# Kernel tuning notes

Hardware: AMD Instinct MI355X
Metric: run time of the kernel (lower is better)

## Reference

```python
import jax, jax.numpy as jnp
import numpy as np
import math

NUM_HEADS = 16
VEC_SIZE = 1024
HEAD_DIM = VEC_SIZE // NUM_HEADS


def setup_inputs() -> dict:
    key = jax.random.key(0)
    k1, k2, k3, k4, k5 = jax.random.split(key, 5)
    B, S, D = 2, 2048, VEC_SIZE
    x = jax.random.normal(k1, (B, S, D), dtype=jnp.float32)
    # Linear params, torch-style: y = x @ W.T + b
    s1 = 1.0 / math.sqrt(D)
    W_qkv = jax.random.uniform(k2, (3 * D, D), minval=-s1, maxval=s1, dtype=jnp.float32)
    b_qkv = jax.random.uniform(k3, (3 * D,), minval=-s1, maxval=s1, dtype=jnp.float32)
    W_out = jax.random.uniform(k4, (D, D), minval=-s1, maxval=s1, dtype=jnp.float32)
    b_out = jax.random.uniform(k5, (D,), minval=-s1, maxval=s1, dtype=jnp.float32)
    return {"x": x, "W_qkv": W_qkv, "b_qkv": b_qkv, "W_out": W_out, "b_out": b_out}


def reference(x, W_qkv, b_qkv, W_out, b_out):
    B, S, D = x.shape
    H, Hd = NUM_HEADS, HEAD_DIM
    qkv = x @ W_qkv.T + b_qkv                      # [B,S,3D]
    q, k, v = jnp.split(qkv, 3, axis=-1)
    # [B,S,H,Hd] -> [B,H,S,Hd]
    q = q.reshape(B, S, H, Hd).transpose(0, 2, 1, 3)
    k = k.reshape(B, S, H, Hd).transpose(0, 2, 1, 3)
    v = v.reshape(B, S, H, Hd).transpose(0, 2, 1, 3)
    weight = jnp.einsum('bhqd,bhkd->bhqk', q, k)   # [B,H,S,S]
    causal = jnp.triu(jnp.ones((S, S), dtype=bool), k=1)
    weight = jnp.where(causal, -jnp.inf, weight)
    weight = weight / jnp.sqrt(jnp.asarray(Hd, dtype=weight.dtype))
    weight = jax.nn.softmax(weight, axis=-1)
    out = jnp.einsum('bhqk,bhkd->bhqd', weight, v)  # [B,H,S,Hd]
    out = out.transpose(0, 2, 1, 3).reshape(B, S, D)
    return out @ W_out.T + b_out
```

## Files before the change

kernel.cpp:

```cpp
#include <hip/hip_runtime.h>
#include <hip/hip_bf16.h>

typedef __attribute__((ext_vector_type(8))) short short8;
typedef __attribute__((ext_vector_type(4))) short s4v;
typedef __attribute__((ext_vector_type(4))) float floatx4;

__device__ inline floatx4 mfma_bf16(short8 a, short8 b, floatx4 c) {
  return __builtin_amdgcn_mfma_f32_16x16x32_bf16(a, b, c, 0, 0, 0);
}
__device__ inline float exp2_fast(float x) { return __builtin_amdgcn_exp2f(x); }

__device__ inline short bf16s(float f) {
  __hip_bfloat16 h = __float2bfloat16(f);
  return *reinterpret_cast<short*>(&h);
}
__device__ inline float sbf16(short s) {
  return __bfloat162float(*reinterpret_cast<__hip_bfloat16*>(&s));
}

__device__ inline void gld16(__hip_bfloat16* lds, const __hip_bfloat16* g) {
  __builtin_amdgcn_global_load_lds(
      (const __attribute__((address_space(1))) void*)g,
      (__attribute__((address_space(3))) void*)lds, 16, 0, 0);
}

__global__ __launch_bounds__(256) void cvt_all(
    const float* __restrict__ x, const float* __restrict__ wqkv,
    const float* __restrict__ wout, __hip_bfloat16* __restrict__ xb,
    __hip_bfloat16* __restrict__ wqkvb, __hip_bfloat16* __restrict__ wob) {
  const int n1 = 4194304, n2 = 3145728;
  int i = (blockIdx.x * 256 + threadIdx.x) * 8;
  const float* src;
  __hip_bfloat16* dst;
  int off;
  if (i < n1) { src = x; dst = xb; off = i; }
  else if (i < n1 + n2) { src = wqkv; dst = wqkvb; off = i - n1; }
  else { src = wout; dst = wob; off = i - n1 - n2; }
  float4 a = *reinterpret_cast<const float4*>(src + off);
  float4 b = *reinterpret_cast<const float4*>(src + off + 4);
  __hip_bfloat16 t[8];
  t[0] = __float2bfloat16(a.x); t[1] = __float2bfloat16(a.y);
  t[2] = __float2bfloat16(a.z); t[3] = __float2bfloat16(a.w);
  t[4] = __float2bfloat16(b.x); t[5] = __float2bfloat16(b.y);
  t[6] = __float2bfloat16(b.z); t[7] = __float2bfloat16(b.w);
  *reinterpret_cast<short8*>(dst + off) = *reinterpret_cast<short8*>(t);
}

template<int TN, bool OUT_BF16>
__global__ __launch_bounds__(256) void gemm_bt(
    const __hip_bfloat16* __restrict__ A, const __hip_bfloat16* __restrict__ Bt,
    const float* __restrict__ bias, void* __restrict__ Cout,
    int M, int N, int K) {
  __shared__ __align__(16) __hip_bfloat16 As[128 * 64];
  __shared__ __align__(16) __hip_bfloat16 Bs[TN * 64];
  const int tid = threadIdx.x;
  const int wave = tid >> 6, lane = tid & 63, quad = lane >> 4, l15 = lane & 15;
  const int wm = (wave >> 1) * 64, wn = (wave & 1) * (TN / 2);
  const int m0 = blockIdx.y * 128, n0 = blockIdx.x * TN;
  const int NC = TN / 32;

  floatx4 acc[4][NC];
  for (int r = 0; r < 4; ++r)
    for (int c = 0; c < NC; ++c) acc[r][c] = (floatx4){0.f, 0.f, 0.f, 0.f};

  for (int k0 = 0; k0 < K; k0 += 64) {
    __syncthreads();
    for (int it = 0; it < 4; ++it) {
      int idx = it * 256 + tid;
      int row = idx >> 3, col = ((idx & 7) ^ (row & 7)) * 8;
      gld16(&As[idx * 8], A + (size_t)(m0 + row) * K + k0 + col);
    }
    for (int it = 0; it < TN * 64 / 2048; ++it) {
      int idx = it * 256 + tid;
      int row = idx >> 3, col = ((idx & 7) ^ (row & 7)) * 8;
      gld16(&Bs[idx * 8], Bt + (size_t)(n0 + row) * K + k0 + col);
    }
    __syncthreads();
    for (int ks = 0; ks < 2; ++ks) {
      short8 af[4], bf[NC];
      for (int r = 0; r < 4; ++r) {
        int row = wm + r * 16 + l15;
        af[r] = *reinterpret_cast<const short8*>(
            &As[row * 64 + (((ks * 4 + quad) ^ (l15 & 7)) * 8)]);
      }
      for (int c = 0; c < NC; ++c) {
        int row = wn + c * 16 + l15;
        bf[c] = *reinterpret_cast<const short8*>(
            &Bs[row * 64 + (((ks * 4 + quad) ^ (l15 & 7)) * 8)]);
      }
      for (int r = 0; r < 4; ++r)
        for (int c = 0; c < NC; ++c)
          acc[r][c] = mfma_bf16(af[r], bf[c], acc[r][c]);
    }
  }

  for (int c = 0; c < NC; ++c) {
    int gn = n0 + wn + c * 16 + l15;
    float bv = bias[gn];
    for (int r = 0; r < 4; ++r)
      for (int rg = 0; rg < 4; ++rg) {
        int gm = m0 + wm + r * 16 + quad * 4 + rg;
        float v = acc[r][c][rg] + bv;
        if (OUT_BF16)
          ((__hip_bfloat16*)Cout)[(size_t)gm * N + gn] = __float2bfloat16(v);
        else
          ((float*)Cout)[(size_t)gm * N + gn] = v;
      }
  }
}

__device__ inline void stage_half(__hip_bfloat16* lds, const __hip_bfloat16* g,
                                  int K, int tid) {
#pragma unroll
  for (int it = 0; it < 2; ++it) {
    int idx = it * 512 + tid;
    int row = idx >> 3, col = ((idx & 7) ^ (row & 7)) * 8;
    gld16(lds + idx * 8, g + (size_t)row * K + col);
  }
}

#define VMW(N) asm volatile("s_waitcnt vmcnt(" #N ")" ::: "memory")
#define LGKM0 asm volatile("s_waitcnt lgkmcnt(0)" ::: "memory")
#define BAR __builtin_amdgcn_s_barrier()

#define LDA8(dst, BUF, MH)                                                     \
  do {                                                                         \
    _Pragma("unroll") for (int mf = 0; mf < 4; ++mf) {                         \
      int rh = wm * 64 + mf * 16 + l15;                                        \
      _Pragma("unroll") for (int ks = 0; ks < 2; ++ks)                         \
          dst[mf][ks] = *reinterpret_cast<const short8*>(                      \
              &SA[BUF][MH][rh * 64 + (((ks * 4 + quad) ^ (rh & 7)) * 8)]);     \
    }                                                                          \
  } while (0)
#define LDB4(dst, BUF, NH)                                                     \
  do {                                                                         \
    _Pragma("unroll") for (int nf = 0; nf < 2; ++nf) {                         \
      int rh = wn * 32 + nf * 16 + l15;                                        \
      _Pragma("unroll") for (int ks = 0; ks < 2; ++ks)                         \
          dst[nf][ks] = *reinterpret_cast<const short8*>(                      \
              &SB[BUF][NH][rh * 64 + (((ks * 4 + quad) ^ (rh & 7)) * 8)]);     \
    }                                                                          \
  } while (0)
#define MM16(MH, NH, AF, BF)                                                   \
  do {                                                                         \
    _Pragma("unroll") for (int mf = 0; mf < 4; ++mf)                           \
        _Pragma("unroll") for (int nf = 0; nf < 2; ++nf) {                     \
      acc[MH][NH][mf][nf] = mfma_bf16(AF[mf][0], BF[nf][0], acc[MH][NH][mf][nf]); \
      acc[MH][NH][mf][nf] = mfma_bf16(AF[mf][1], BF[nf][1], acc[MH][NH][mf][nf]); \
    }                                                                          \
  } while (0)
#define PH(RD, STG, MH, NH, AF, BF, WT)                                        \
  do {                                                                         \
    RD;                                                                        \
    STG;                                                                       \
    BAR;                                                                       \
    __builtin_amdgcn_s_setprio(1);                                             \
    MM16(MH, NH, AF, BF);                                                      \
    __builtin_amdgcn_s_setprio(0);                                             \
    WT;                                                                        \
    LGKM0;                                                                     \
    BAR;                                                                       \
  } while (0)

template<bool OUT_BF16>
__global__ __launch_bounds__(512, 2) void gemm_256(
    const __hip_bfloat16* __restrict__ A, const __hip_bfloat16* __restrict__ Bt,
    const float* __restrict__ bias, void* __restrict__ Cout,
    int M, int N, int K) {
  __shared__ __align__(16) __hip_bfloat16 SA[2][2][128 * 64];
  __shared__ __align__(16) __hip_bfloat16 SB[2][2][128 * 64];
  const int tid = threadIdx.x;
  const int lane = tid & 63, quad = (lane >> 4), l15 = lane & 15;
  const int wave = tid >> 6;
  const int wm = wave >> 2, wn = wave & 3;

  const int nbx = gridDim.x;
  int bid = blockIdx.y * nbx + blockIdx.x;
  const int nwg = nbx * gridDim.y;
  if ((nwg & 7) == 0) bid = (bid & 7) * (nwg >> 3) + (bid >> 3);
  const int bx = bid % nbx, by = bid / nbx;
  const int m0 = by * 256, n0 = bx * 256;

  const __hip_bfloat16* Abase = A + (size_t)m0 * K;
  const __hip_bfloat16* Bbase = Bt + (size_t)n0 * K;
  const int NT = K >> 6;

  floatx4 acc[2][2][4][2];
#pragma unroll
  for (int a = 0; a < 2; ++a)
#pragma unroll
    for (int b = 0; b < 2; ++b)
#pragma unroll
      for (int c = 0; c < 4; ++c)
#pragma unroll
        for (int d = 0; d < 2; ++d) acc[a][b][c][d] = (floatx4){0.f, 0.f, 0.f, 0.f};

  short8 af0[4][2], af1[4][2];
  short8 bf0c[2][2], bf0n[2][2];
  short8 bf1[2][2];

  stage_half(&SB[0][0][0], Bbase, K, tid);
  stage_half(&SA[0][0][0], Abase, K, tid);
  stage_half(&SB[0][1][0], Bbase + (size_t)128 * K, K, tid);
  stage_half(&SA[0][1][0], Abase + (size_t)128 * K, K, tid);
  stage_half(&SB[1][0][0], Bbase + 64, K, tid);
  stage_half(&SA[1][0][0], Abase + 64, K, tid);
  stage_half(&SB[1][1][0], Bbase + (size_t)128 * K + 64, K, tid);
  stage_half(&SA[1][1][0], Abase + (size_t)128 * K + 64, K, tid);
  VMW(12);
  BAR;
  LDB4(bf0c, 0, 0);
  LDA8(af0, 0, 0);
  VMW(10);
  LGKM0;
  BAR;

  for (int t = 0; t <= NT - 3; ++t) {
    const int cb = t & 1, nb = cb ^ 1;
    const size_t k2 = (size_t)(t + 2) * 64;
    PH(LDB4(bf1, cb, 1), stage_half(&SB[cb][0][0], Bbase + k2, K, tid),
       0, 0, af0, bf0c, VMW(10));
    PH(LDA8(af1, cb, 1), stage_half(&SA[cb][0][0], Abase + k2, K, tid),
       0, 1, af0, bf1, VMW(10));
    PH(LDB4(bf0n, nb, 0),
       stage_half(&SB[cb][1][0], Bbase + (size_t)128 * K + k2, K, tid),
       1, 1, af1, bf1, VMW(10));
    PH(LDA8(af0, nb, 0),
       stage_half(&SA[cb][1][0], Abase + (size_t)128 * K + k2, K, tid),
       1, 0, af1, bf0c, VMW(10));
#pragma unroll
    for (int nf = 0; nf < 2; ++nf)
#pragma unroll
      for (int ks = 0; ks < 2; ++ks) bf0c[nf][ks] = bf0n[nf][ks];
  }
  {
    const int cb = (NT - 2) & 1, nb = cb ^ 1;
    PH(LDB4(bf1, cb, 1), (void)0, 0, 0, af0, bf0c, VMW(8));
    PH(LDA8(af1, cb, 1), (void)0, 0, 1, af0, bf1, VMW(6));
    PH(LDB4(bf0n, nb, 0), (void)0, 1, 1, af1, bf1, VMW(4));
    PH(LDA8(af0, nb, 0), (void)0, 1, 0, af1, bf0c, VMW(2));
#pragma unroll
    for (int nf = 0; nf < 2; ++nf)
#pragma unroll
      for (int ks = 0; ks < 2; ++ks) bf0c[nf][ks] = bf0n[nf][ks];
  }
  {
    const int cb = (NT - 1) & 1;
    PH(LDB4(bf1, cb, 1), (void)0, 0, 0, af0, bf0c, VMW(0));
    PH(LDA8(af1, cb, 1), (void)0, 0, 1, af0, bf1, (void)0);
    __builtin_amdgcn_s_setprio(1);
    MM16(1, 1, af1, bf1);
    MM16(1, 0, af1, bf0c);
    __builtin_amdgcn_s_setprio(0);
  }

#pragma unroll
  for (int nh = 0; nh < 2; ++nh)
#pragma unroll
    for (int nf = 0; nf < 2; ++nf) {
      int gn = n0 + nh * 128 + wn * 32 + nf * 16 + l15;
      float bv = bias[gn];
#pragma unroll
      for (int mh = 0; mh < 2; ++mh)
#pragma unroll
        for (int mf = 0; mf < 4; ++mf)
#pragma unroll
          for (int rg = 0; rg < 4; ++rg) {
            int gm = m0 + mh * 128 + wm * 64 + mf * 16 + quad * 4 + rg;
            float v = acc[mh][nh][mf][nf][rg] + bv;
            if (OUT_BF16)
              ((__hip_bfloat16*)Cout)[(size_t)gm * N + gn] = __float2bfloat16(v);
            else
              ((float*)Cout)[(size_t)gm * N + gn] = v;
          }
    }
}

__global__ __launch_bounds__(256, 4) void flash_attn(
    const __hip_bfloat16* __restrict__ qkv, __hip_bfloat16* __restrict__ out) {
  const int S = 2048, QKV = 3072;
  const int bx = blockIdx.x;
  const int g = (blockIdx.y >> 3) + 2 * blockIdx.z;
  int qt;
  if (g == 0)      qt = bx;
  else if (g == 1) qt = 31 - bx;
  else if (g == 2) qt = (bx + 8) & 31;
  else             qt = (23 - bx) & 31;
  const int h = blockIdx.y, b = blockIdx.z;
  const int q0 = qt * 64;
  __shared__ __align__(16) short Ps[2][64 * 64];
  const int tid = threadIdx.x;
  const int wave = tid >> 6, lane = tid & 63, quad = lane >> 4, l15 = lane & 15;
  const int rx = l15 & 7;
  const __hip_bfloat16* base = qkv + (size_t)b * S * QKV;
  const float c2 = 0.18033688011112042f;
  const floatx4 zero4 = {0.f, 0.f, 0.f, 0.f};
  const int krow = 16 * wave + l15;

  const __hip_bfloat16* kbase = base + 1024 + h * 64;
  const __hip_bfloat16* vbase = base + 2048 + h * 64;

  for (int it = 0; it < 2; ++it) {
    int v = tid + it * 256;
    int row = v >> 3, cb = v & 7;
    int colp = (cb ^ (row & 7)) * 8;
    short8 qv = *reinterpret_cast<const short8*>(
        base + (size_t)(q0 + row) * QKV + h * 64 + cb * 8);
    short qs[8];
    for (int e = 0; e < 8; ++e) qs[e] = bf16s(sbf16(qv[e]) * c2);
    *reinterpret_cast<short8*>(&Ps[1][row * 64 + colp]) = *reinterpret_cast<short8*>(qs);
  }
  short8 kA0 = *reinterpret_cast<const short8*>(
      kbase + (size_t)krow * QKV + quad * 8);
  short8 kA1 = *reinterpret_cast<const short8*>(
      kbase + (size_t)krow * QKV + 32 + quad * 8);
  __syncthreads();

  short8 aq[4][2];
  for (int t4 = 0; t4 < 4; ++t4)
    for (int s = 0; s < 2; ++s)
      aq[t4][s] = *reinterpret_cast<const short8*>(
          &Ps[1][(t4 * 16 + l15) * 64 + (((s * 4 + quad) ^ rx) * 8)]);

  floatx4 o_acc[4];
  for (int m = 0; m < 4; ++m) o_acc[m] = zero4;
  float lsum4[4] = {0.f, 0.f, 0.f, 0.f};
  short8 vA0, vA1;

  for (int j = 0; j <= qt; ++j) {
    const int cj = j & 1, pj = cj ^ 1;

    short8 kB0, kB1, vB0, vB1;
    if (j < qt) {
      const __hip_bfloat16* kp = kbase + (size_t)((j + 1) * 64 + krow) * QKV;
      kB0 = *reinterpret_cast<const short8*>(kp + quad * 8);
      kB1 = *reinterpret_cast<const short8*>(kp + 32 + quad * 8);
    }
    {
      const __hip_bfloat16* vp = vbase + (size_t)(j * 64 + quad * 8) * QKV + krow;
      for (int i = 0; i < 8; ++i) {
        vB0[i] = *reinterpret_cast<const short*>(vp + (size_t)i * QKV);
        vB1[i] = *reinterpret_cast<const short*>(vp + (size_t)(32 + i) * QKV);
      }
    }

    if (j > 0) {
      for (int s = 0; s < 2; ++s) {
        short8 bv = s ? vA1 : vA0;
        for (int m = 0; m < 4; ++m) {
          short8 ap = *reinterpret_cast<const short8*>(
              &Ps[pj][(m * 16 + l15) * 64 + (((4 * s + quad) ^ rx) * 8)]);
          o_acc[m] = mfma_bf16(ap, bv, o_acc[m]);
        }
      }
    }

    floatx4 sc[4];
    for (int t4 = 0; t4 < 4; ++t4) {
      sc[t4] = mfma_bf16(kA0, aq[t4][0], zero4);
      sc[t4] = mfma_bf16(kA1, aq[t4][1], sc[t4]);
    }
    if (j == qt) {
      int kloc = 16 * wave + quad * 4;
      for (int t4 = 0; t4 < 4; ++t4)
        for (int rg = 0; rg < 4; ++rg)
          if (kloc + rg > t4 * 16 + l15) sc[t4][rg] = -1e30f;
    }

    const int pcol = ((2 * wave + (quad >> 1)) ^ rx) * 8 + (quad & 1) * 4;
    for (int t4 = 0; t4 < 4; ++t4) {
      short pp[4];
      for (int rg = 0; rg < 4; ++rg) {
        float p = exp2_fast(sc[t4][rg]);
        lsum4[t4] += p;
        pp[rg] = bf16s(p);
      }
      *reinterpret_cast<s4v*>(&Ps[cj][(t4 * 16 + l15) * 64 + pcol]) =
          *reinterpret_cast<s4v*>(pp);
    }

    kA0 = kB0; kA1 = kB1; vA0 = vB0; vA1 = vB1;
    __syncthreads();
  }

  const int pq = qt & 1;
  for (int s = 0; s < 2; ++s) {
    short8 bv = s ? vA1 : vA0;
    for (int m = 0; m < 4; ++m) {
      short8 ap = *reinterpret_cast<const short8*>(
          &Ps[pq][(m * 16 + l15) * 64 + (((4 * s + quad) ^ rx) * 8)]);
      o_acc[m] = mfma_bf16(ap, bv, o_acc[m]);
    }
  }
  for (int t4 = 0; t4 < 4; ++t4) {
    lsum4[t4] += __shfl_xor(lsum4[t4], 16);
    lsum4[t4] += __shfl_xor(lsum4[t4], 32);
  }
  float* Lf = (float*)&Ps[pq ^ 1][0];
  if (quad == 0)
    for (int t4 = 0; t4 < 4; ++t4)
      Lf[wave * 64 + t4 * 16 + l15] = lsum4[t4];
  __syncthreads();
  if (tid < 64)
    Lf[256 + tid] = 1.0f / (Lf[tid] + Lf[64 + tid] + Lf[128 + tid] + Lf[192 + tid]);
  __syncthreads();

  const int dcol = h * 64 + krow;
  for (int m = 0; m < 4; ++m)
    for (int rg = 0; rg < 4; ++rg) {
      int q = m * 16 + quad * 4 + rg;
      out[(size_t)(b * S + q0 + q) * 1024 + dcol] =
          __float2bfloat16(o_acc[m][rg] * Lf[256 + q]);
    }
}

extern "C" void kernel_launch(void* const* d_in, const int* in_sizes, int n_in,
                              void* d_out, int out_size, void* d_ws, size_t ws_size,
                              hipStream_t stream) {
  const float* x    = (const float*)d_in[0];
  const float* Wqkv = (const float*)d_in[1];
  const float* bqkv = (const float*)d_in[2];
  const float* Wout = (const float*)d_in[3];
  const float* bout = (const float*)d_in[4];
  float* out = (float*)d_out;

  const int BS = 2 * 2048;
  const int D = 1024;
  char* ws = (char*)d_ws;
  __hip_bfloat16* xb    = (__hip_bfloat16*)(ws);
  __hip_bfloat16* wqkvb = (__hip_bfloat16*)(ws + (size_t)8  * 1048576);
  __hip_bfloat16* wob   = (__hip_bfloat16*)(ws + (size_t)14 * 1048576);
  __hip_bfloat16* qkvb  = (__hip_bfloat16*)(ws + (size_t)16 * 1048576);
  __hip_bfloat16* attnb = (__hip_bfloat16*)(ws + (size_t)40 * 1048576);

  cvt_all<<<4096, 256, 0, stream>>>(x, Wqkv, Wout, xb, wqkvb, wob);

  gemm_256<true><<<dim3(3072 / 256, BS / 256), 512, 0, stream>>>(
      xb, wqkvb, bqkv, qkvb, BS, 3 * D, D);

  flash_attn<<<dim3(32, 16, 2), 256, 0, stream>>>(qkvb, attnb);

  gemm_bt<64, false><<<dim3(1024 / 64, BS / 128), 256, 0, stream>>>(
      attnb, wob, bout, out, BS, D, D);
}
```

Baseline: 197.6 us.

## Reorder GEMM phase schedule to load fragments per tile and drop lgkm waits

Measured after the change: 173.7 us. 12.1% less time.

```diff
diff --git a/kernel.cpp b/kernel.cpp
--- a/kernel.cpp
+++ b/kernel.cpp
@@ -120,7 +120,6 @@
 }
 
 #define VMW(N) asm volatile("s_waitcnt vmcnt(" #N ")" ::: "memory")
-#define LGKM0 asm volatile("s_waitcnt lgkmcnt(0)" ::: "memory")
 #define BAR __builtin_amdgcn_s_barrier()
 
 #define LDA8(dst, BUF, MH)                                                     \
@@ -158,7 +157,6 @@
     MM16(MH, NH, AF, BF);                                                      \
     __builtin_amdgcn_s_setprio(0);                                             \
     WT;                                                                        \
-    LGKM0;                                                                     \
     BAR;                                                                       \
   } while (0)
 
@@ -196,61 +194,50 @@
         for (int d = 0; d < 2; ++d) acc[a][b][c][d] = (floatx4){0.f, 0.f, 0.f, 0.f};
 
   short8 af0[4][2], af1[4][2];
-  short8 bf0c[2][2], bf0n[2][2];
-  short8 bf1[2][2];
-
+  short8 bf0[2][2], bf1[2][2];
+
+  stage_half(&SA[0][0][0], Abase, K, tid);
   stage_half(&SB[0][0][0], Bbase, K, tid);
-  stage_half(&SA[0][0][0], Abase, K, tid);
+  stage_half(&SA[0][1][0], Abase + (size_t)128 * K, K, tid);
   stage_half(&SB[0][1][0], Bbase + (size_t)128 * K, K, tid);
-  stage_half(&SA[0][1][0], Abase + (size_t)128 * K, K, tid);
+  stage_half(&SA[1][0][0], Abase + 64, K, tid);
   stage_half(&SB[1][0][0], Bbase + 64, K, tid);
-  stage_half(&SA[1][0][0], Abase + 64, K, tid);
+  stage_half(&SA[1][1][0], Abase + (size_t)128 * K + 64, K, tid);
   stage_half(&SB[1][1][0], Bbase + (size_t)128 * K + 64, K, tid);
-  stage_half(&SA[1][1][0], Abase + (size_t)128 * K + 64, K, tid);
   VMW(12);
   BAR;
-  LDB4(bf0c, 0, 0);
-  LDA8(af0, 0, 0);
-  VMW(10);
-  LGKM0;
-  BAR;
 
   for (int t = 0; t <= NT - 3; ++t) {
-    const int cb = t & 1, nb = cb ^ 1;
+    const int cb = t & 1;
     const size_t k2 = (size_t)(t + 2) * 64;
-    PH(LDB4(bf1, cb, 1), stage_half(&SB[cb][0][0], Bbase + k2, K, tid),
-       0, 0, af0, bf0c, VMW(10));
-    PH(LDA8(af1, cb, 1), stage_half(&SA[cb][0][0], Abase + k2, K, tid),
-       0, 1, af0, bf1, VMW(10));
-    PH(LDB4(bf0n, nb, 0),
+    PH({ LDA8(af0, cb, 0); LDB4(bf0, cb, 0); }, (void)0,
+       0, 0, af0, bf0, VMW(10));
+    PH(LDA8(af1, cb, 1),
+       { stage_half(&SA[cb][0][0], Abase + k2, K, tid);
+         stage_half(&SB[cb][0][0], Bbase + k2, K, tid); },
+       1, 0, af1, bf0, VMW(12));
+    PH(LDB4(bf1, cb, 1),
+       stage_half(&SA[cb][1][0], Abase + (size_t)128 * K + k2, K, tid),
+       1, 1, af1, bf1, (void)0);
+    PH((void)0,
        stage_half(&SB[cb][1][0], Bbase + (size_t)128 * K + k2, K, tid),
-       1, 1, af1, bf1, VMW(10));
-    PH(LDA8(af0, nb, 0),
-       stage_half(&SA[cb][1][0], Abase + (size_t)128 * K + k2, K, tid),
-       1, 0, af1, bf0c, VMW(10));
-#pragma unroll
-    for (int nf = 0; nf < 2; ++nf)
-#pragma unroll
-      for (int ks = 0; ks < 2; ++ks) bf0c[nf][ks] = bf0n[nf][ks];
+       0, 1, af0, bf1, VMW(12));
   }
   {
-    const int cb = (NT - 2) & 1, nb = cb ^ 1;
-    PH(LDB4(bf1, cb, 1), (void)0, 0, 0, af0, bf0c, VMW(8));
-    PH(LDA8(af1, cb, 1), (void)0, 0, 1, af0, bf1, VMW(6));
-    PH(LDB4(bf0n, nb, 0), (void)0, 1, 1, af1, bf1, VMW(4));
-    PH(LDA8(af0, nb, 0), (void)0, 1, 0, af1, bf0c, VMW(2));
-#pragma unroll
-    for (int nf = 0; nf < 2; ++nf)
-#pragma unroll
-      for (int ks = 0; ks < 2; ++ks) bf0c[nf][ks] = bf0n[nf][ks];
+    const int cb = (NT - 2) & 1;
+    PH({ LDA8(af0, cb, 0); LDB4(bf0, cb, 0); }, (void)0, 0, 0, af0, bf0, VMW(10));
+    PH(LDA8(af1, cb, 1), (void)0, 1, 0, af1, bf0, VMW(8));
+    PH(LDB4(bf1, cb, 1), (void)0, 1, 1, af1, bf1, (void)0);
+    PH((void)0, (void)0, 0, 1, af0, bf1, VMW(4));
   }
   {
     const int cb = (NT - 1) & 1;
-    PH(LDB4(bf1, cb, 1), (void)0, 0, 0, af0, bf0c, VMW(0));
-    PH(LDA8(af1, cb, 1), (void)0, 0, 1, af0, bf1, (void)0);
+    PH({ LDA8(af0, cb, 0); LDB4(bf0, cb, 0); }, (void)0, 0, 0, af0, bf0, VMW(2));
+    PH(LDA8(af1, cb, 1), (void)0, 1, 0, af1, bf0, VMW(0));
+    LDB4(bf1, cb, 1);
     __builtin_amdgcn_s_setprio(1);
     MM16(1, 1, af1, bf1);
-    MM16(1, 0, af1, bf0c);
+    MM16(0, 1, af0, bf1);
     __builtin_amdgcn_s_setprio(0);
   }
 
```
